# Kernel optimization log

Hardware: AMD Instinct MI355X
Metric: run time of the kernel (lower is better)

The kernel has to match this reference:

```python
import jax, jax.numpy as jnp
import numpy as np

N = 10000
E = 320000
IN_DIM = 256
HID = 128
HEADS = 3
NEG_SLOPE = 0.2
EPS = 1e-8


def setup_inputs() -> dict:
    key = jax.random.key(0)
    ks = jax.random.split(key, 12)
    rn = lambda k, s, sc=0.1: jax.random.normal(k, s, dtype=jnp.float32) * sc
    return {
        'x1': jax.random.normal(ks[0], (N, IN_DIM), dtype=jnp.float32),
        'edge_index1': jax.random.randint(ks[1], (2, E), 0, N, dtype=jnp.int64),
        'x2': jax.random.normal(ks[2], (N, IN_DIM), dtype=jnp.float32),
        'edge_index2': jax.random.randint(ks[3], (2, E), 0, N, dtype=jnp.int64),
        'W1': rn(ks[4], (IN_DIM, HEADS * HID)),
        'att_src1': rn(ks[5], (HEADS, HID)),
        'att_dst1': rn(ks[6], (HEADS, HID)),
        'b1': rn(ks[7], (HEADS * HID,)),
        'W2': rn(ks[8], (HEADS * HID, HID)),
        'att_src2': rn(ks[9], (1, HID)),
        'att_dst2': rn(ks[10], (1, HID)),
        'b2': rn(ks[11], (HID,)),
    }


def gat_conv(x, edge_index, W, a_src, a_dst, bias, heads, out_ch, concat):
    """PyG-style GATConv with add_self_loops=True."""
    n = x.shape[0]
    loops = jnp.arange(n, dtype=edge_index.dtype)
    ei = jnp.concatenate([edge_index, jnp.stack([loops, loops])], axis=1)
    src, dst = ei[0], ei[1]
    h = (x @ W).reshape(n, heads, out_ch)                    # [N,H,C]
    s = jnp.einsum('nhc,hc->nh', h, a_src)                    # alpha_src per node
    d = jnp.einsum('nhc,hc->nh', h, a_dst)                    # alpha_dst per node
    e = jax.nn.leaky_relu(s[src] + d[dst], NEG_SLOPE)         # [Etot,H]
    m = jax.ops.segment_max(e, dst, num_segments=n)           # segment softmax (stable)
    ex = jnp.exp(e - m[dst])
    denom = jax.ops.segment_sum(ex, dst, num_segments=n)
    alpha = ex / denom[dst]                                   # [Etot,H]
    out = jax.ops.segment_sum(h[src] * alpha[:, :, None], dst, num_segments=n)
    out = out.reshape(n, heads * out_ch) if concat else out.mean(axis=1)
    return out + bias, (ei, alpha)


def _branch(x, ei, W1, as1, ad1, b1, W2, as2, ad2, b2):
    e1, (ei_sl, alpha1) = gat_conv(x, ei, W1, as1, ad1, b1, HEADS, HID, True)
    e1 = jax.nn.relu(e1)
    e2, _ = gat_conv(e1, ei, W2, as2, ad2, b2, 1, HID, False)
    # _graph_pooling
    attn_val = alpha1.mean(axis=1)                            # [Etot]
    node_attn = jax.ops.segment_sum(attn_val, ei_sl[1], num_segments=x.shape[0])
    weighted = e2 * node_attn[:, None]
    pooled = jnp.concatenate([weighted.mean(axis=0), e2.mean(axis=0)])  # [2*HID]
    return pooled, alpha1


def reference(x1, edge_index1, x2, edge_index2, W1, att_src1, att_dst1, b1,
              W2, att_src2, att_dst2, b2):
    g1, alpha1 = _branch(x1, edge_index1, W1, att_src1, att_dst1, b1,
                         W2, att_src2, att_dst2, b2)
    g2, alpha2 = _branch(x2, edge_index2, W1, att_src1, att_dst1, b1,
                         W2, att_src2, att_dst2, b2)
    n1 = jnp.maximum(jnp.linalg.norm(g1), EPS)
    n2 = jnp.maximum(jnp.linalg.norm(g2), EPS)
    sim = jnp.dot(g1, g2) / (n1 * n2)
    return sim, alpha1, alpha2
```

## Files before the change

kernel.cpp:

```cpp
#include <hip/hip_runtime.h>
#include <hip/hip_bf16.h>
#include <cstdint>
#include <cstddef>

#define INDIM 256
#define NEG 0.2f

typedef __attribute__((ext_vector_type(8))) short short8v;
typedef __attribute__((ext_vector_type(4))) float f32x4;
typedef __attribute__((ext_vector_type(2))) float f32x2;

__device__ __forceinline__ unsigned short f2bf(float x) {
  __hip_bfloat16 b = __float2bfloat16(x);
  return __builtin_bit_cast(unsigned short, b);
}

__device__ __forceinline__ unsigned char f2fp8(float v) {
  int packed = __builtin_amdgcn_cvt_pk_fp8_f32(v, v, 0, false);
  return (unsigned char)(packed & 0xff);
}

__device__ __forceinline__ float lrelu(float v) { return v > 0.f ? v : NEG * v; }

__global__ void wprep_kernel(const float* __restrict__ W1, __hip_bfloat16* __restrict__ W1t,
                             const float* __restrict__ W2, __hip_bfloat16* __restrict__ W2t) {
  int idx = blockIdx.x * blockDim.x + threadIdx.x;
  const int T1 = 256 * 384;
  if (idx < T1) {
    int k = idx / 384, c = idx - k * 384;
    W1t[(size_t)c * 256 + k] = __float2bfloat16(W1[idx]);
  } else {
    int i = idx - T1;
    if (i < 384 * 128) {
      int k = i / 128, c = i - k * 128;
      W2t[(size_t)c * 384 + k] = __float2bfloat16(W2[i]);
    }
  }
}

template<int K, bool ABF16, int NH>
__global__ __launch_bounds__(256) void mfma_gemm(const void* __restrict__ A0,
                                                 const void* __restrict__ A1, int Nsplit,
                                                 const __hip_bfloat16* __restrict__ Wt,
                                                 const float* __restrict__ att_s,
                                                 const float* __restrict__ att_d,
                                                 unsigned char* __restrict__ Yc,
                                                 float* __restrict__ So,
                                                 float* __restrict__ Do,
                                                 int M, int NC) {
  constexpr int SST = (NH == 3) ? 4 : 1;
  __shared__ short As[64][40];
  __shared__ short Bs[128][40];
  __shared__ float sred[2][64];
  const int tid = threadIdx.x;
  const int row0 = blockIdx.x * 64;
  const int col0 = blockIdx.y * 128;
  const int l = tid & 63, w = tid >> 6;
  const int wr = w >> 1, wc = w & 1;
  const int lr = l & 15, lk = (l >> 4) * 8;

  f32x4 acc[2][4];
#pragma unroll
  for (int m = 0; m < 2; ++m)
#pragma unroll
    for (int n = 0; n < 4; ++n) acc[m][n] = {0.f, 0.f, 0.f, 0.f};

  for (int k0 = 0; k0 < K; k0 += 32) {
    __syncthreads();
    {
      int r = tid >> 2, kq = (tid & 3) * 8;
      int gr = row0 + r;
      short8v av = {0, 0, 0, 0, 0, 0, 0, 0};
      if (gr < M) {
        const void* Ab = (gr < Nsplit) ? A0 : A1;
        int lrow = (gr < Nsplit) ? gr : gr - Nsplit;
        if (ABF16) {
          av = *(const short8v*)((const short*)Ab + (size_t)lrow * K + k0 + kq);
        } else {
          const float* ap = (const float*)Ab + (size_t)lrow * K + k0 + kq;
          float4 u = *(const float4*)ap;
          float4 v = *(const float4*)(ap + 4);
          av = short8v{(short)f2bf(u.x), (short)f2bf(u.y), (short)f2bf(u.z), (short)f2bf(u.w),
                       (short)f2bf(v.x), (short)f2bf(v.y), (short)f2bf(v.z), (short)f2bf(v.w)};
        }
      }
      *(short8v*)&As[r][kq] = av;
    }
    {
      int c = tid >> 1, kq = (tid & 1) * 8;
      const short* wp = (const short*)Wt + (size_t)(col0 + c) * K + k0 + kq;
      *(short8v*)&Bs[c][kq]      = *(const short8v*)wp;
      *(short8v*)&Bs[c][kq + 16] = *(const short8v*)(wp + 16);
    }
    __syncthreads();
    short8v a[2], b[4];
#pragma unroll
    for (int m = 0; m < 2; ++m) a[m] = *(short8v*)&As[wr * 32 + m * 16 + lr][lk];
#pragma unroll
    for (int n = 0; n < 4; ++n) b[n] = *(short8v*)&Bs[wc * 64 + n * 16 + lr][lk];
#pragma unroll
    for (int m = 0; m < 2; ++m)
#pragma unroll
      for (int n = 0; n < 4; ++n)
        acc[m][n] = __builtin_amdgcn_mfma_f32_16x16x32_bf16(a[m], b[n], acc[m][n], 0, 0, 0);
  }
#pragma unroll
  for (int m = 0; m < 2; ++m) {
    int rbase = row0 + wr * 32 + m * 16 + (l >> 4) * 4;
#pragma unroll
    for (int n = 0; n < 4; ++n) {
      int col = col0 + wc * 64 + n * 16 + lr;
#pragma unroll
      for (int q = 0; q < 4; ++q) {
        int row = rbase + q;
        if (row < M) Yc[(size_t)row * NC + col] = f2fp8(acc[m][n][q]);
      }
    }
  }
  float asv[4], adv[4];
#pragma unroll
  for (int n = 0; n < 4; ++n) {
    int col = col0 + wc * 64 + n * 16 + lr;
    asv[n] = att_s[col];
    adv[n] = att_d[col];
  }
  float ps[2][4], pd[2][4];
#pragma unroll
  for (int m = 0; m < 2; ++m)
#pragma unroll
    for (int q = 0; q < 4; ++q) {
      float s = 0.f, d = 0.f;
#pragma unroll
      for (int n = 0; n < 4; ++n) {
        s = fmaf(acc[m][n][q], asv[n], s);
        d = fmaf(acc[m][n][q], adv[n], d);
      }
      ps[m][q] = s; pd[m][q] = d;
    }
#pragma unroll
  for (int o = 1; o < 16; o <<= 1) {
#pragma unroll
    for (int m = 0; m < 2; ++m)
#pragma unroll
      for (int q = 0; q < 4; ++q) {
        ps[m][q] += __shfl_xor(ps[m][q], o);
        pd[m][q] += __shfl_xor(pd[m][q], o);
      }
  }
  __syncthreads();
  if (wc == 1 && lr == 0) {
#pragma unroll
    for (int m = 0; m < 2; ++m)
#pragma unroll
      for (int q = 0; q < 4; ++q) {
        int rl = wr * 32 + m * 16 + (l >> 4) * 4 + q;
        sred[0][rl] = ps[m][q];
        sred[1][rl] = pd[m][q];
      }
  }
  __syncthreads();
  if (wc == 0 && lr == 0) {
#pragma unroll
    for (int m = 0; m < 2; ++m)
#pragma unroll
      for (int q = 0; q < 4; ++q) {
        int rl = wr * 32 + m * 16 + (l >> 4) * 4 + q;
        int row = row0 + rl;
        if (row < M) {
          So[(size_t)row * SST + blockIdx.y] = ps[m][q] + sred[0][rl];
          Do[(size_t)row * SST + blockIdx.y] = pd[m][q] + sred[1][rl];
        }
      }
  }
}

__global__ void deg_kernel(const int* __restrict__ ed1, const int* __restrict__ ed2,
                           int E, int Etot, int N, int* __restrict__ deg) {
  int idx = blockIdx.x * blockDim.x + threadIdx.x;
  if (idx >= 2 * Etot) return;
  int br = idx >= Etot;
  int el = idx - br * Etot;
  const int* ed = br ? ed2 : ed1;
  int dn = ((el < E) ? ed[el] : (el - E)) + br * N;
  atomicAdd(&deg[dn], 1);
}

__global__ __launch_bounds__(1024) void scan_kernel(const int* __restrict__ deg,
                                                    int* __restrict__ rowptr,
                                                    int* __restrict__ cursor, int n) {
  __shared__ int wsum[16];
  int t = threadIdx.x, lane = t & 63, wid = t >> 6;
  int start = t * 20;
  int v[20];
  int s = 0;
#pragma unroll
  for (int k = 0; k < 20; ++k) {
    int i = start + k;
    int d = (i < n) ? deg[i] : 0;
    s += d;
    v[k] = s;
  }
  int x = s;
#pragma unroll
  for (int o = 1; o < 64; o <<= 1) {
    int tm = __shfl_up(x, o);
    if (lane >= o) x += tm;
  }
  if (lane == 63) wsum[wid] = x;
  __syncthreads();
  if (wid == 0) {
    int wv = (lane < 16) ? wsum[lane] : 0;
#pragma unroll
    for (int o = 1; o < 16; o <<= 1) {
      int tm = __shfl_up(wv, o);
      if (lane >= o) wv += tm;
    }
    if (lane < 16) wsum[lane] = wv;
  }
  __syncthreads();
  int excl = (x - s) + (wid ? wsum[wid - 1] : 0);
  if (t == 0) rowptr[0] = 0;
#pragma unroll
  for (int k = 0; k < 20; ++k) {
    int i = start + k;
    if (i < n) {
      rowptr[i + 1] = excl + v[k];
      cursor[i] = excl + (k ? v[k - 1] : 0);
    }
  }
}

__global__ void fill_kernel(const int* __restrict__ es1, const int* __restrict__ ed1,
                            const int* __restrict__ es2, const int* __restrict__ ed2,
                            int E, int Etot, int N, int* __restrict__ cursor,
                            int* __restrict__ csr_src) {
  int idx = blockIdx.x * blockDim.x + threadIdx.x;
  if (idx >= 2 * Etot) return;
  int br = idx >= Etot;
  int el = idx - br * Etot;
  const int* es = br ? es2 : es1;
  const int* ed = br ? ed2 : ed1;
  int sn, dn;
  if (el < E) { sn = es[el]; dn = ed[el]; } else { sn = dn = el - E; }
  sn += br * N; dn += br * N;
  int pos = atomicAdd(&cursor[dn], 1);
  csr_src[pos] = sn;
}

__global__ __launch_bounds__(256) void agg1_kernel(const unsigned char* __restrict__ h1c,
                                                   const float* __restrict__ S4,
                                                   const float* __restrict__ D4,
                                                   const int* __restrict__ rowptr,
                                                   const int* __restrict__ csr_src,
                                                   const float* __restrict__ b1,
                                                   __hip_bfloat16* __restrict__ e1b,
                                                   float* __restrict__ invden, int N2) {
  __shared__ float4 st[4][64];
  int wv = threadIdx.x >> 6;
  int n = blockIdx.x * 4 + wv;
  if (n >= N2) return;
  int l = threadIdx.x & 63;
  int head = l >> 5;
  const float4* S4v = reinterpret_cast<const float4*>(S4);
  int p0 = rowptr[n], p1 = rowptr[n + 1];
  float d0 = D4[n * 4], d1 = D4[n * 4 + 1], d2 = D4[n * 4 + 2];

  float dp0 = 0.f, dp1 = 0.f, dp2 = 0.f;
  float acc[6] = {0.f, 0.f, 0.f, 0.f, 0.f, 0.f};
  for (int base = p0; base < p1; base += 64) {
    int cnt = min(64, p1 - base);
    if (l < cnt) {
      int sn = csr_src[base + l];
      float4 sv = S4v[sn];
      float e0 = __expf(lrelu(sv.x + d0));
      float e1 = __expf(lrelu(sv.y + d1));
      float e2 = __expf(lrelu(sv.z + d2));
      st[wv][l] = make_float4(__int_as_float(sn), e0, e1, e2);
      dp0 += e0; dp1 += e1; dp2 += e2;
    }
    int i = 0;
    for (; i + 4 <= cnt; i += 4) {
      float4 w[4];
      unsigned int hv[4];
      unsigned short gv[4];
#pragma unroll
      for (int u = 0; u < 4; ++u) {
        w[u] = st[wv][i + u];
        int sn = __float_as_int(w[u].x);
        const unsigned char* row = h1c + (size_t)sn * 384;
        hv[u] = *reinterpret_cast<const unsigned int*>(row + 4 * l);
        gv[u] = *reinterpret_cast<const unsigned short*>(row + 256 + 2 * l);
      }
#pragma unroll
      for (int u = 0; u < 4; ++u) {
        float alo = head ? w[u].z : w[u].y;
        float ahi = w[u].w;
        f32x2 f0 = __builtin_amdgcn_cvt_pk_f32_fp8((int)hv[u], false);
        f32x2 f1 = __builtin_amdgcn_cvt_pk_f32_fp8((int)hv[u], true);
        f32x2 g0 = __builtin_amdgcn_cvt_pk_f32_fp8((int)(unsigned int)gv[u], false);
        acc[0] = fmaf(alo, f0.x, acc[0]);
        acc[1] = fmaf(alo, f0.y, acc[1]);
        acc[2] = fmaf(alo, f1.x, acc[2]);
        acc[3] = fmaf(alo, f1.y, acc[3]);
        acc[4] = fmaf(ahi, g0.x, acc[4]);
        acc[5] = fmaf(ahi, g0.y, acc[5]);
      }
    }
    for (; i < cnt; ++i) {
      float4 w = st[wv][i];
      int sn = __float_as_int(w.x);
      const unsigned char* row = h1c + (size_t)sn * 384;
      unsigned int hv = *reinterpret_cast<const unsigned int*>(row + 4 * l);
      unsigned short gv = *reinterpret_cast<const unsigned short*>(row + 256 + 2 * l);
      float alo = head ? w.z : w.y;
      float ahi = w.w;
      f32x2 f0 = __builtin_amdgcn_cvt_pk_f32_fp8((int)hv, false);
      f32x2 f1 = __builtin_amdgcn_cvt_pk_f32_fp8((int)hv, true);
      f32x2 g0 = __builtin_amdgcn_cvt_pk_f32_fp8((int)(unsigned int)gv, false);
      acc[0] = fmaf(alo, f0.x, acc[0]);
      acc[1] = fmaf(alo, f0.y, acc[1]);
      acc[2] = fmaf(alo, f1.x, acc[2]);
      acc[3] = fmaf(alo, f1.y, acc[3]);
      acc[4] = fmaf(ahi, g0.x, acc[4]);
      acc[5] = fmaf(ahi, g0.y, acc[5]);
    }
  }
#pragma unroll
  for (int o = 32; o; o >>= 1) {
    dp0 += __shfl_down(dp0, o); dp1 += __shfl_down(dp1, o); dp2 += __shfl_down(dp2, o);
  }
  float inv0 = 1.f / __shfl(dp0, 0);
  float inv1 = 1.f / __shfl(dp1, 0);
  float inv2 = 1.f / __shfl(dp2, 0);

  float ilo = head ? inv1 : inv0;
  int c0 = 4 * l;
  float4 bb = *reinterpret_cast<const float4*>(b1 + c0);
  float v0 = acc[0] * ilo + bb.x;
  float v1 = acc[1] * ilo + bb.y;
  float v2 = acc[2] * ilo + bb.z;
  float v3 = acc[3] * ilo + bb.w;
  v0 = v0 > 0.f ? v0 : 0.f; v1 = v1 > 0.f ? v1 : 0.f;
  v2 = v2 > 0.f ? v2 : 0.f; v3 = v3 > 0.f ? v3 : 0.f;
  int ch = 256 + 2 * l;
  float2 bh = *reinterpret_cast<const float2*>(b1 + ch);
  float v4 = acc[4] * inv2 + bh.x;
  float v5 = acc[5] * inv2 + bh.y;
  v4 = v4 > 0.f ? v4 : 0.f; v5 = v5 > 0.f ? v5 : 0.f;
  unsigned short* eb = reinterpret_cast<unsigned short*>(e1b) + (size_t)n * 384;
  uint2 lo;
  lo.x = (unsigned int)f2bf(v0) | ((unsigned int)f2bf(v1) << 16);
  lo.y = (unsigned int)f2bf(v2) | ((unsigned int)f2bf(v3) << 16);
  *reinterpret_cast<uint2*>(eb + c0) = lo;
  *reinterpret_cast<unsigned int*>(eb + ch) =
      (unsigned int)f2bf(v4) | ((unsigned int)f2bf(v5) << 16);
  if (l == 0) invden[n * 3] = inv0;
  else if (l == 1) invden[n * 3 + 1] = inv1;
  else if (l == 2) invden[n * 3 + 2] = inv2;
}

__global__ void alpha_kernel(const float* __restrict__ S4, const float* __restrict__ D4,
                             const float* __restrict__ invden,
                             const int* __restrict__ es1, const int* __restrict__ ed1,
                             const int* __restrict__ es2, const int* __restrict__ ed2,
                             int E, int Etot, int N, float* __restrict__ out) {
  int idx = blockIdx.x * blockDim.x + threadIdx.x;
  if (idx >= 2 * Etot) return;
  int br = idx >= Etot;
  int el = idx - br * Etot;
  const int* es = br ? es2 : es1;
  const int* ed = br ? ed2 : ed1;
  int sn, dn;
  if (el < E) { sn = es[el]; dn = ed[el]; } else { sn = dn = el - E; }
  sn += br * N; dn += br * N;
  float* ao = out + 1 + (size_t)br * Etot * 3 + (size_t)el * 3;
#pragma unroll
  for (int h = 0; h < 3; ++h) {
    float v = lrelu(S4[sn * 4 + h] + D4[dn * 4 + h]);
    ao[h] = __expf(v) * invden[dn * 3 + h];
  }
}

__global__ __launch_bounds__(256) void agg2_kernel(const unsigned char* __restrict__ h2c,
                                                   const float* __restrict__ S2,
                                                   const float* __restrict__ D2,
                                                   const int* __restrict__ rowptr,
                                                   const int* __restrict__ csr_src,
                                                   const float* __restrict__ b2,
                                                   float* __restrict__ e2out, int N2) {
  __shared__ int lsrc[4][256];
  __shared__ float la[4][256];
  const unsigned int* H4 = reinterpret_cast<const unsigned int*>(h2c);
  int wv = threadIdx.x >> 6;
  int n = blockIdx.x * 4 + wv;
  if (n >= N2) return;
  int lane = threadIdx.x & 63;
  int half = lane >> 5, t = lane & 31;
  int p0 = rowptr[n], p1 = rowptr[n + 1];
  float dnv = D2[n];

  float dpart = 0.f;
  float acc[4] = {0.f, 0.f, 0.f, 0.f};
  for (int base = p0; base < p1; base += 256) {
    int cnt = min(256, p1 - base);
    for (int i = lane; i < cnt; i += 64) {
      int sn = csr_src[base + i];
      lsrc[wv][i] = sn;
      float ex = __expf(lrelu(S2[sn] + dnv));
      la[wv][i] = ex;
      dpart += ex;
    }
    int i = half;
    for (; i + 14 < cnt; i += 16) {
      unsigned int hv[8];
      float av[8];
#pragma unroll
      for (int u = 0; u < 8; ++u) {
        int e = i + 2 * u;
        int sn = lsrc[wv][e];
        av[u] = la[wv][e];
        hv[u] = H4[(size_t)sn * 32 + t];
      }
#pragma unroll
      for (int u = 0; u < 8; ++u) {
        f32x2 f0 = __builtin_amdgcn_cvt_pk_f32_fp8((int)hv[u], false);
        f32x2 f1 = __builtin_amdgcn_cvt_pk_f32_fp8((int)hv[u], true);
        acc[0] = fmaf(av[u], f0.x, acc[0]);
        acc[1] = fmaf(av[u], f0.y, acc[1]);
        acc[2] = fmaf(av[u], f1.x, acc[2]);
        acc[3] = fmaf(av[u], f1.y, acc[3]);
      }
    }
    for (; i < cnt; i += 2) {
      int sn = lsrc[wv][i];
      float a = la[wv][i];
      unsigned int hv = H4[(size_t)sn * 32 + t];
      f32x2 f0 = __builtin_amdgcn_cvt_pk_f32_fp8((int)hv, false);
      f32x2 f1 = __builtin_amdgcn_cvt_pk_f32_fp8((int)hv, true);
      acc[0] = fmaf(a, f0.x, acc[0]);
      acc[1] = fmaf(a, f0.y, acc[1]);
      acc[2] = fmaf(a, f1.x, acc[2]);
      acc[3] = fmaf(a, f1.y, acc[3]);
    }
  }
#pragma unroll
  for (int k = 0; k < 4; ++k) acc[k] += __shfl_xor(acc[k], 32);
#pragma unroll
  for (int o = 32; o; o >>= 1) dpart += __shfl_down(dpart, o);
  float invden = 1.f / __shfl(dpart, 0);
  if (half == 0) {
    float4 bb = *reinterpret_cast<const float4*>(b2 + 4 * t);
    float4 ov;
    ov.x = acc[0] * invden + bb.x;
    ov.y = acc[1] * invden + bb.y;
    ov.z = acc[2] * invden + bb.z;
    ov.w = acc[3] * invden + bb.w;
    *reinterpret_cast<float4*>(e2out + (size_t)n * 128 + 4 * t) = ov;
  }
}

__global__ __launch_bounds__(128) void pool_kernel(const float* __restrict__ e2,
                                                   float* __restrict__ g, int N, float invN) {
  int c = threadIdx.x;
  int br = blockIdx.y;
  int r0 = br * N + blockIdx.x * 128;
  int r1 = min(r0 + 128, br * N + N);
  float acc = 0.f;
  for (int n = r0; n < r1; ++n) acc += e2[(size_t)n * 128 + c];
  atomicAdd(&g[br * 128 + c], acc * invN);
}

__global__ __launch_bounds__(128) void sim_kernel(const float* __restrict__ g1,
                                                  const float* __restrict__ g2,
                                                  float* __restrict__ out) {
  int t = threadIdx.x;
  float a = g1[t], b = g2[t];
  __shared__ float sd[128], s1[128], s2[128];
  sd[t] = a * b; s1[t] = a * a; s2[t] = b * b;
  __syncthreads();
  for (int ofs = 64; ofs; ofs >>= 1) {
    if (t < ofs) { sd[t] += sd[t + ofs]; s1[t] += s1[t + ofs]; s2[t] += s2[t + ofs]; }
    __syncthreads();
  }
  if (t == 0) {
    float n1 = fmaxf(sqrtf(s1[0]), 1e-8f);
    float n2 = fmaxf(sqrtf(s2[0]), 1e-8f);
    out[0] = sd[0] / (n1 * n2);
  }
}

extern "C" void kernel_launch(void* const* d_in, const int* in_sizes, int n_in,
                              void* d_out, int out_size, void* d_ws, size_t ws_size,
                              hipStream_t stream) {
  const int N = in_sizes[0] / INDIM;
  const int E = in_sizes[1] / 2;
  const int Etot = E + N;
  const int N2 = 2 * N;

  const float* x1  = (const float*)d_in[0];
  const int*   ei1 = (const int*)d_in[1];
  const float* x2  = (const float*)d_in[2];
  const int*   ei2 = (const int*)d_in[3];
  const float* W1  = (const float*)d_in[4];
  const float* as1 = (const float*)d_in[5];
  const float* ad1 = (const float*)d_in[6];
  const float* b1  = (const float*)d_in[7];
  const float* W2  = (const float*)d_in[8];
  const float* as2 = (const float*)d_in[9];
  const float* ad2 = (const float*)d_in[10];
  const float* b2  = (const float*)d_in[11];
  float* out = (float*)d_out;
  const int* es1 = ei1, *ed1 = ei1 + E;
  const int* es2 = ei2, *ed2 = ei2 + E;

  char* p = (char*)d_ws;
  auto alloc = [&](size_t bytes) -> char* {
    char* q = p;
    p += (bytes + 255) & ~(size_t)255;
    return q;
  };
  unsigned char* h1c = (unsigned char*)alloc((size_t)N2 * 384);
  __hip_bfloat16* e1b = (__hip_bfloat16*)alloc((size_t)N2 * 384 * 2);
  unsigned char* h2c = (unsigned char*)alloc((size_t)N2 * 128);
  float* e2          = (float*)alloc((size_t)N2 * 128 * 4);
  __hip_bfloat16* W1t = (__hip_bfloat16*)alloc((size_t)256 * 384 * 2);
  __hip_bfloat16* W2t = (__hip_bfloat16*)alloc((size_t)384 * 128 * 2);
  float* s1v  = (float*)alloc((size_t)N2 * 4 * 4);
  float* d1v  = (float*)alloc((size_t)N2 * 4 * 4);
  float* s2v  = (float*)alloc((size_t)N2 * 4);
  float* d2v  = (float*)alloc((size_t)N2 * 4);
  float* idn  = (float*)alloc((size_t)N2 * 3 * 4);
  float* g    = (float*)alloc(256 * 4);
  int* deg     = (int*)alloc((size_t)N2 * 4);
  int* rowptr  = (int*)alloc((size_t)(N2 + 1) * 4);
  int* cursor  = (int*)alloc((size_t)N2 * 4);
  int* csr_src = (int*)alloc((size_t)2 * Etot * 4);

  const int EB = 256;
  const int egrid2 = (2 * Etot + EB - 1) / EB;
  const int gmx = (N2 + 63) / 64;

  hipMemsetAsync(g, 0, 256 * 4, stream);
  hipMemsetAsync(deg, 0, (size_t)N2 * 4, stream);
  wprep_kernel<<<(256 * 384 + 384 * 128 + 255) / 256, 256, 0, stream>>>(W1, W1t, W2, W2t);

  deg_kernel<<<egrid2, EB, 0, stream>>>(ed1, ed2, E, Etot, N, deg);
  mfma_gemm<256, false, 3><<<dim3(gmx, 3), 256, 0, stream>>>(x1, x2, N, W1t, as1, ad1,
                                                             h1c, s1v, d1v, N2, 384);
  scan_kernel<<<1, 1024, 0, stream>>>(deg, rowptr, cursor, N2);
  fill_kernel<<<egrid2, EB, 0, stream>>>(es1, ed1, es2, ed2, E, Etot, N, cursor, csr_src);

  agg1_kernel<<<(N2 + 3) / 4, 256, 0, stream>>>(h1c, s1v, d1v, rowptr, csr_src, b1,
                                                e1b, idn, N2);

  mfma_gemm<384, true, 1><<<dim3(gmx, 1), 256, 0, stream>>>(e1b, e1b, N2, W2t, as2, ad2,
                                                            h2c, s2v, d2v, N2, 128);
  alpha_kernel<<<egrid2, EB, 0, stream>>>(s1v, d1v, idn, es1, ed1, es2, ed2, E, Etot, N, out);
  agg2_kernel<<<(N2 + 3) / 4, 256, 0, stream>>>(h2c, s2v, d2v, rowptr, csr_src, b2, e2, N2);

  pool_kernel<<<dim3((N + 127) / 128, 2), 128, 0, stream>>>(e2, g, N, 1.f / (float)N);
  sim_kernel<<<1, 128, 0, stream>>>(g, g + 128, out);
}
```

Baseline: 234.5 us.

## Co-launch independent kernels as heterogeneous blocks and fuse pooling with similarity

Merges the degree-count kernel into the first GEMM launch and the alpha kernel into the second GEMM launch by giving each fused kernel two kinds of blocks selected by block index. The pool and cosine-similarity kernels are combined using a last-block-done atomic counter, and the two memsets become one contiguous zeroing of the counter, pooled vector and degree buffers. The aim is to cut launch count and let independent work fill the GPU at the same time. In exchange the fused kernels all use the GEMM's shared-memory footprint, and the final reduction depends on threadfence and atomic ordering.

```diff
diff --git a/kernel.cpp b/kernel.cpp
--- a/kernel.cpp
+++ b/kernel.cpp
@@ -38,23 +38,22 @@
   }
 }
 
-template<int K, bool ABF16, int NH>
-__global__ __launch_bounds__(256) void mfma_gemm(const void* __restrict__ A0,
-                                                 const void* __restrict__ A1, int Nsplit,
-                                                 const __hip_bfloat16* __restrict__ Wt,
-                                                 const float* __restrict__ att_s,
-                                                 const float* __restrict__ att_d,
-                                                 unsigned char* __restrict__ Yc,
-                                                 float* __restrict__ So,
-                                                 float* __restrict__ Do,
-                                                 int M, int NC) {
-  constexpr int SST = (NH == 3) ? 4 : 1;
-  __shared__ short As[64][40];
-  __shared__ short Bs[128][40];
-  __shared__ float sred[2][64];
+template<int K, bool ABF16, int SST>
+__device__ __forceinline__ void gemm_body(int bx, int by,
+                                          const void* __restrict__ A0,
+                                          const void* __restrict__ A1, int Nsplit,
+                                          const __hip_bfloat16* __restrict__ Wt,
+                                          const float* __restrict__ att_s,
+                                          const float* __restrict__ att_d,
+                                          unsigned char* __restrict__ Yc,
+                                          float* __restrict__ So,
+                                          float* __restrict__ Do,
+                                          int M, int NC,
+                                          short (*As)[40], short (*Bs)[40],
+                                          float (*sred)[64]) {
   const int tid = threadIdx.x;
-  const int row0 = blockIdx.x * 64;
-  const int col0 = blockIdx.y * 128;
+  const int row0 = bx * 64;
+  const int col0 = by * 128;
   const int l = tid & 63, w = tid >> 6;
   const int wr = w >> 1, wc = w & 1;
   const int lr = l & 15, lk = (l >> 4) * 8;
@@ -167,22 +166,87 @@
         int rl = wr * 32 + m * 16 + (l >> 4) * 4 + q;
         int row = row0 + rl;
         if (row < M) {
-          So[(size_t)row * SST + blockIdx.y] = ps[m][q] + sred[0][rl];
-          Do[(size_t)row * SST + blockIdx.y] = pd[m][q] + sred[1][rl];
+          So[(size_t)row * SST + by] = ps[m][q] + sred[0][rl];
+          Do[(size_t)row * SST + by] = pd[m][q] + sred[1][rl];
         }
       }
   }
 }
 
-__global__ void deg_kernel(const int* __restrict__ ed1, const int* __restrict__ ed2,
-                           int E, int Etot, int N, int* __restrict__ deg) {
-  int idx = blockIdx.x * blockDim.x + threadIdx.x;
-  if (idx >= 2 * Etot) return;
-  int br = idx >= Etot;
-  int el = idx - br * Etot;
-  const int* ed = br ? ed2 : ed1;
-  int dn = ((el < E) ? ed[el] : (el - E)) + br * N;
-  atomicAdd(&deg[dn], 1);
+__global__ __launch_bounds__(256) void gemm1_deg_kernel(const float* __restrict__ x1,
+                                                        const float* __restrict__ x2, int Nsplit,
+                                                        const __hip_bfloat16* __restrict__ Wt,
+                                                        const float* __restrict__ att_s,
+                                                        const float* __restrict__ att_d,
+                                                        unsigned char* __restrict__ Yc,
+                                                        float* __restrict__ So,
+                                                        float* __restrict__ Do,
+                                                        int M, int gmx,
+                                                        const int* __restrict__ ed1,
+                                                        const int* __restrict__ ed2,
+                                                        int E, int Etot, int N,
+                                                        int* __restrict__ deg) {
+  __shared__ short As[64][40];
+  __shared__ short Bs[128][40];
+  __shared__ float sred[2][64];
+  int bid = blockIdx.x;
+  if (bid < gmx * 3) {
+    gemm_body<256, false, 4>(bid % gmx, bid / gmx, x1, x2, Nsplit, Wt, att_s, att_d,
+                             Yc, So, Do, M, 384, As, Bs, sred);
+  } else {
+    int idx = (bid - gmx * 3) * 256 + threadIdx.x;
+    if (idx < 2 * Etot) {
+      int br = idx >= Etot;
+      int el = idx - br * Etot;
+      const int* ed = br ? ed2 : ed1;
+      int dn = ((el < E) ? ed[el] : (el - E)) + br * N;
+      atomicAdd(&deg[dn], 1);
+    }
+  }
+}
+
+__global__ __launch_bounds__(256) void gemm2_alpha_kernel(const __hip_bfloat16* __restrict__ e1b,
+                                                          const __hip_bfloat16* __restrict__ Wt,
+                                                          const float* __restrict__ att_s,
+                                                          const float* __restrict__ att_d,
+                                                          unsigned char* __restrict__ Yc,
+                                                          float* __restrict__ So,
+                                                          float* __restrict__ Do,
+                                                          int M, int gmx,
+                                                          const float* __restrict__ S4,
+                                                          const float* __restrict__ D4,
+                                                          const float* __restrict__ invden,
+                                                          const int* __restrict__ es1,
+                                                          const int* __restrict__ ed1,
+                                                          const int* __restrict__ es2,
+                                                          const int* __restrict__ ed2,
+                                                          int E, int Etot, int N,
+                                                          float* __restrict__ out) {
+  __shared__ short As[64][40];
+  __shared__ short Bs[128][40];
+  __shared__ float sred[2][64];
+  int bid = blockIdx.x;
+  if (bid < gmx) {
+    gemm_body<384, true, 1>(bid, 0, e1b, e1b, M, Wt, att_s, att_d,
+                            Yc, So, Do, M, 128, As, Bs, sred);
+  } else {
+    int idx = (bid - gmx) * 256 + threadIdx.x;
+    if (idx < 2 * Etot) {
+      int br = idx >= Etot;
+      int el = idx - br * Etot;
+      const int* es = br ? es2 : es1;
+      const int* ed = br ? ed2 : ed1;
+      int sn, dn;
+      if (el < E) { sn = es[el]; dn = ed[el]; } else { sn = dn = el - E; }
+      sn += br * N; dn += br * N;
+      float* ao = out + 1 + (size_t)br * Etot * 3 + (size_t)el * 3;
+#pragma unroll
+      for (int h = 0; h < 3; ++h) {
+        float v = lrelu(S4[sn * 4 + h] + D4[dn * 4 + h]);
+        ao[h] = __expf(v) * invden[dn * 3 + h];
+      }
+    }
+  }
 }
 
 __global__ __launch_bounds__(1024) void scan_kernel(const int* __restrict__ deg,
@@ -359,28 +423,6 @@
   else if (l == 2) invden[n * 3 + 2] = inv2;
 }
 
-__global__ void alpha_kernel(const float* __restrict__ S4, const float* __restrict__ D4,
-                             const float* __restrict__ invden,
-                             const int* __restrict__ es1, const int* __restrict__ ed1,
-                             const int* __restrict__ es2, const int* __restrict__ ed2,
-                             int E, int Etot, int N, float* __restrict__ out) {
-  int idx = blockIdx.x * blockDim.x + threadIdx.x;
-  if (idx >= 2 * Etot) return;
-  int br = idx >= Etot;
-  int el = idx - br * Etot;
-  const int* es = br ? es2 : es1;
-  const int* ed = br ? ed2 : ed1;
-  int sn, dn;
-  if (el < E) { sn = es[el]; dn = ed[el]; } else { sn = dn = el - E; }
-  sn += br * N; dn += br * N;
-  float* ao = out + 1 + (size_t)br * Etot * 3 + (size_t)el * 3;
-#pragma unroll
-  for (int h = 0; h < 3; ++h) {
-    float v = lrelu(S4[sn * 4 + h] + D4[dn * 4 + h]);
-    ao[h] = __expf(v) * invden[dn * 3 + h];
-  }
-}
-
 __global__ __launch_bounds__(256) void agg2_kernel(const unsigned char* __restrict__ h2c,
                                                    const float* __restrict__ S2,
                                                    const float* __restrict__ D2,
@@ -459,8 +501,11 @@
   }
 }
 
-__global__ __launch_bounds__(128) void pool_kernel(const float* __restrict__ e2,
-                                                   float* __restrict__ g, int N, float invN) {
+__global__ __launch_bounds__(128) void pool_sim_kernel(const float* __restrict__ e2,
+                                                       float* __restrict__ g,
+                                                       int* __restrict__ cnt,
+                                                       int N, float invN,
+                                                       float* __restrict__ out) {
   int c = threadIdx.x;
   int br = blockIdx.y;
   int r0 = br * N + blockIdx.x * 128;
@@ -468,21 +513,24 @@
   float acc = 0.f;
   for (int n = r0; n < r1; ++n) acc += e2[(size_t)n * 128 + c];
   atomicAdd(&g[br * 128 + c], acc * invN);
-}
-
-__global__ __launch_bounds__(128) void sim_kernel(const float* __restrict__ g1,
-                                                  const float* __restrict__ g2,
-                                                  float* __restrict__ out) {
-  int t = threadIdx.x;
-  float a = g1[t], b = g2[t];
+  __threadfence();
+  __shared__ bool last;
   __shared__ float sd[128], s1[128], s2[128];
-  sd[t] = a * b; s1[t] = a * a; s2[t] = b * b;
+  if (c == 0) {
+    int total = gridDim.x * gridDim.y;
+    last = (atomicAdd(cnt, 1) == total - 1);
+  }
+  __syncthreads();
+  if (!last) return;
+  float a = atomicAdd(&g[c], 0.f);
+  float b = atomicAdd(&g[128 + c], 0.f);
+  sd[c] = a * b; s1[c] = a * a; s2[c] = b * b;
   __syncthreads();
   for (int ofs = 64; ofs; ofs >>= 1) {
-    if (t < ofs) { sd[t] += sd[t + ofs]; s1[t] += s1[t + ofs]; s2[t] += s2[t + ofs]; }
+    if (c < ofs) { sd[c] += sd[c + ofs]; s1[c] += s1[c + ofs]; s2[c] += s2[c + ofs]; }
     __syncthreads();
   }
-  if (t == 0) {
+  if (c == 0) {
     float n1 = fmaxf(sqrtf(s1[0]), 1e-8f);
     float n2 = fmaxf(sqrtf(s2[0]), 1e-8f);
     out[0] = sd[0] / (n1 * n2);
@@ -519,6 +567,11 @@
     p += (bytes + 255) & ~(size_t)255;
     return q;
   };
+  float* g   = (float*)alloc(256 * 4);
+  int*   cnt = (int*)alloc(256);
+  int*   deg = (int*)alloc((size_t)N2 * 4);
+  size_t zero_bytes = (size_t)((char*)deg - (char*)g) + (((size_t)N2 * 4 + 255) & ~(size_t)255);
+
   unsigned char* h1c = (unsigned char*)alloc((size_t)N2 * 384);
   __hip_bfloat16* e1b = (__hip_bfloat16*)alloc((size_t)N2 * 384 * 2);
   unsigned char* h2c = (unsigned char*)alloc((size_t)N2 * 128);
@@ -530,8 +583,6 @@
   float* s2v  = (float*)alloc((size_t)N2 * 4);
   float* d2v  = (float*)alloc((size_t)N2 * 4);
   float* idn  = (float*)alloc((size_t)N2 * 3 * 4);
-  float* g    = (float*)alloc(256 * 4);
-  int* deg     = (int*)alloc((size_t)N2 * 4);
   int* rowptr  = (int*)alloc((size_t)(N2 + 1) * 4);
   int* cursor  = (int*)alloc((size_t)N2 * 4);
   int* csr_src = (int*)alloc((size_t)2 * Etot * 4);
@@ -540,24 +591,24 @@
   const int egrid2 = (2 * Etot + EB - 1) / EB;
   const int gmx = (N2 + 63) / 64;
 
-  hipMemsetAsync(g, 0, 256 * 4, stream);
-  hipMemsetAsync(deg, 0, (size_t)N2 * 4, stream);
+  hipMemsetAsync(g, 0, zero_bytes, stream);
   wprep_kernel<<<(256 * 384 + 384 * 128 + 255) / 256, 256, 0, stream>>>(W1, W1t, W2, W2t);
 
-  deg_kernel<<<egrid2, EB, 0, stream>>>(ed1, ed2, E, Etot, N, deg);
-  mfma_gemm<256, false, 3><<<dim3(gmx, 3), 256, 0, stream>>>(x1, x2, N, W1t, as1, ad1,
-                                                             h1c, s1v, d1v, N2, 384);
+  gemm1_deg_kernel<<<gmx * 3 + egrid2, 256, 0, stream>>>(x1, x2, N, W1t, as1, ad1,
+                                                         h1c, s1v, d1v, N2, gmx,
+                                                         ed1, ed2, E, Etot, N, deg);
   scan_kernel<<<1, 1024, 0, stream>>>(deg, rowptr, cursor, N2);
   fill_kernel<<<egrid2, EB, 0, stream>>>(es1, ed1, es2, ed2, E, Etot, N, cursor, csr_src);
 
   agg1_kernel<<<(N2 + 3) / 4, 256, 0, stream>>>(h1c, s1v, d1v, rowptr, csr_src, b1,
                                                 e1b, idn, N2);
 
-  mfma_gemm<384, true, 1><<<dim3(gmx, 1), 256, 0, stream>>>(e1b, e1b, N2, W2t, as2, ad2,
-                                                            h2c, s2v, d2v, N2, 128);
-  alpha_kernel<<<egrid2, EB, 0, stream>>>(s1v, d1v, idn, es1, ed1, es2, ed2, E, Etot, N, out);
+  gemm2_alpha_kernel<<<gmx + egrid2, 256, 0, stream>>>(e1b, W2t, as2, ad2,
+                                                       h2c, s2v, d2v, N2, gmx,
+                                                       s1v, d1v, idn,
+                                                       es1, ed1, es2, ed2, E, Etot, N, out);
   agg2_kernel<<<(N2 + 3) / 4, 256, 0, stream>>>(h2c, s2v, d2v, rowptr, csr_src, b2, e2, N2);
 
-  pool_kernel<<<dim3((N + 127) / 128, 2), 128, 0, stream>>>(e2, g, N, 1.f / (float)N);
-  sim_kernel<<<1, 128, 0, stream>>>(g, g + 128, out);
-}
+  pool_sim_kernel<<<dim3((N + 127) / 128, 2), 128, 0, stream>>>(e2, g, cnt, N,
+                                                                1.f / (float)N, out);
+}
```

After: 220.8 us (median of 3 runs). 5.9% less time.
